# Performance work log

Hardware: AMD Instinct MI355X
Metric: run time of the kernel (lower is better)

The kernel has to match this reference:

```python
import jax, jax.numpy as jnp
import numpy as np
import math

B, S, D, H = 2, 2048, 1024, 16
DK = D // H


def setup_inputs() -> dict:
    key = jax.random.key(0)
    ks = jax.random.split(key, 12)
    s = 1.0 / math.sqrt(D)
    inp = {
        "query": jax.random.normal(ks[0], (B, S, D), jnp.float32),
        "key": jax.random.normal(ks[1], (B, S, D), jnp.float32),
        "value": jax.random.normal(ks[2], (B, S, D), jnp.float32),
        # causal mask, 0 = masked
        "mask": jnp.tril(jnp.ones((S, S), jnp.int32))[None].repeat(B, axis=0),
        "Wq": jax.random.normal(ks[3], (D, D), jnp.float32) * s,
        "bq": jnp.zeros((D,), jnp.float32),
        "Wk": jax.random.normal(ks[4], (D, D), jnp.float32) * s,
        "bk": jnp.zeros((D,), jnp.float32),
        "Wv": jax.random.normal(ks[5], (D, D), jnp.float32) * s,
        "bv": jnp.zeros((D,), jnp.float32),
        "Wo": jax.random.normal(ks[6], (D, D), jnp.float32) * s,
        "bo": jnp.zeros((D,), jnp.float32),
    }
    return inp


def _split_heads(x):
    # [B, S, D] -> [B, H, S, DK]
    b, s, _ = x.shape
    return x.reshape(b, s, H, DK).transpose(0, 2, 1, 3)


def reference(query, key, value, mask, Wq, bq, Wk, bk, Wv, bv, Wo, bo):
    q = _split_heads(query @ Wq + bq)
    k = _split_heads(key @ Wk + bk)
    v = _split_heads(value @ Wv + bv)
    scores = jnp.einsum("bhqd,bhkd->bhqk", q, k) / math.sqrt(DK)
    # mask: [B, Sq, Sk] -> broadcast over heads; 0 entries get -1e9
    scores = jnp.where(mask[:, None, :, :] == 0, jnp.float32(-1e9), scores)
    p = jax.nn.softmax(scores, axis=-1)  # dropout p=0 (eval) -> identity
    x = jnp.einsum("bhqk,bhkd->bhqd", p, v)
    x = x.transpose(0, 2, 1, 3).reshape(query.shape[0], -1, D)
    return x @ Wo + bo
```

## Files before the change

kernel.cpp:

```cpp
#include <hip/hip_runtime.h>
#include <hip/hip_bf16.h>
#include <stdint.h>


constexpr int BATCH = 2, SEQ = 2048, DIM = 1024, NH = 16, HD = 64;
constexpr int MROWS = BATCH * SEQ;

typedef __attribute__((ext_vector_type(4))) float f32x4;
typedef __attribute__((ext_vector_type(8))) short bf16x8;
typedef __attribute__((ext_vector_type(4))) int i32x4;

#define DEVI __device__ __forceinline__

DEVI ushort f2bf(float f) {
  __hip_bfloat16 h = __float2bfloat16(f);
  return __builtin_bit_cast(ushort, h);
}

DEVI f32x4 mfma16(bf16x8 a, bf16x8 b, f32x4 c) {
  return __builtin_amdgcn_mfma_f32_16x16x32_bf16(a, b, c, 0, 0, 0);
}

#if __has_builtin(__builtin_amdgcn_exp2f)
DEVI float fexp2(float x) { return __builtin_amdgcn_exp2f(x); }
#else
DEVI float fexp2(float x) { return exp2f(x); }
#endif

__global__ __launch_bounds__(256) void cvt3(const float* __restrict__ q,
                                            const float* __restrict__ k,
                                            const float* __restrict__ v,
                                            ushort* __restrict__ qo,
                                            ushort* __restrict__ ko,
                                            ushort* __restrict__ vo) {
  const float* src = blockIdx.z == 0 ? q : (blockIdx.z == 1 ? k : v);
  ushort* dst = blockIdx.z == 0 ? qo : (blockIdx.z == 1 ? ko : vo);
  int i = (blockIdx.x * 256 + threadIdx.x) * 4;
  float4 f = *(const float4*)(src + i);
  ushort4 o4 = {f2bf(f.x), f2bf(f.y), f2bf(f.z), f2bf(f.w)};
  *(ushort4*)(dst + i) = o4;
}

__global__ __launch_bounds__(256) void tw(const float* __restrict__ w0,
                                          const float* __restrict__ w1,
                                          const float* __restrict__ w2,
                                          const float* __restrict__ w3,
                                          ushort* __restrict__ t0,
                                          ushort* __restrict__ t1,
                                          ushort* __restrict__ t2,
                                          ushort* __restrict__ t3) {
  const float* W = blockIdx.z == 0 ? w0 : blockIdx.z == 1 ? w1 : blockIdx.z == 2 ? w2 : w3;
  ushort* T = blockIdx.z == 0 ? t0 : blockIdx.z == 1 ? t1 : blockIdx.z == 2 ? t2 : t3;
  __shared__ float tile[32][33];
  int k0 = blockIdx.x * 32, n0 = blockIdx.y * 32;
  int tx = threadIdx.x & 31, ty = threadIdx.x >> 5;
  #pragma unroll
  for (int i = 0; i < 32; i += 8) tile[ty + i][tx] = W[(size_t)(k0 + ty + i) * DIM + n0 + tx];
  __syncthreads();
  #pragma unroll
  for (int i = 0; i < 32; i += 8) T[(size_t)(n0 + ty + i) * DIM + k0 + tx] = f2bf(tile[tx][ty + i]);
}

struct GemmPtrs {
  const ushort* A[3];
  const ushort* Bt[3];
  const float* bias[3];
  void* C[3];
  float scale[3];
};

template <bool F32OUT, bool VT>
__global__ __launch_bounds__(256, 2) void gemm_bt(GemmPtrs gp, int M, int N, int K) {
  const int z = blockIdx.z;
  const ushort* __restrict__ A = gp.A[z];
  const ushort* __restrict__ Bt = gp.Bt[z];
  const float* __restrict__ bias = gp.bias[z];
  const float scale = gp.scale[z];
  const bool vsw = VT && (z == 2);

  __shared__ __align__(16) ushort As[2][128 * 32];
  __shared__ __align__(16) ushort Bs[2][128 * 32];

  const int tid = threadIdx.x;
  const int lane = tid & 63, wv = tid >> 6;
  const int wm = wv >> 1, wn = wv & 1;
  const int l15 = lane & 15, lg = lane >> 4;
  const int m0 = blockIdx.y * 128, n0 = blockIdx.x * 128;

  f32x4 acc[4][4];
  #pragma unroll
  for (int i = 0; i < 4; ++i)
    #pragma unroll
    for (int j = 0; j < 4; ++j) acc[i][j] = f32x4{0.f, 0.f, 0.f, 0.f};

  const int row0 = tid >> 2, k4 = tid & 3;
  const int row1 = row0 + 64;
  const size_t aoff0 = (size_t)(m0 + row0) * K + k4 * 8;
  const size_t aoff1 = (size_t)(m0 + row1) * K + k4 * 8;
  const size_t boff0 = (size_t)(n0 + row0) * K + k4 * 8;
  const size_t boff1 = (size_t)(n0 + row1) * K + k4 * 8;

  i32x4 ra0 = *(const i32x4*)(A + aoff0);
  i32x4 rb0 = *(const i32x4*)(Bt + boff0);
  i32x4 ra1 = *(const i32x4*)(A + aoff1);
  i32x4 rb1 = *(const i32x4*)(Bt + boff1);
  *(i32x4*)&As[0][(size_t)tid * 8] = ra0;
  *(i32x4*)&As[0][(size_t)(256 + tid) * 8] = ra1;
  *(i32x4*)&Bs[0][(size_t)tid * 8] = rb0;
  *(i32x4*)&Bs[0][(size_t)(256 + tid) * 8] = rb1;

  const int nk = K >> 5;
  for (int kt = 0; kt < nk; ++kt) {
    const int cur = kt & 1;
    if (kt + 1 < nk) {
      const int ko = (kt + 1) << 5;
      ra0 = *(const i32x4*)(A + aoff0 + ko);
      rb0 = *(const i32x4*)(Bt + boff0 + ko);
      ra1 = *(const i32x4*)(A + aoff1 + ko);
      rb1 = *(const i32x4*)(Bt + boff1 + ko);
    }
    __syncthreads();

    const ushort* Af = vsw ? &Bs[cur][0] : &As[cur][0];
    const ushort* Bf = vsw ? &As[cur][0] : &Bs[cur][0];
    bf16x8 af[4], bfr[4];
    #pragma unroll
    for (int i = 0; i < 4; ++i) af[i] = *(const bf16x8*)&Af[(wm * 64 + i * 16 + l15) * 32 + lg * 8];
    #pragma unroll
    for (int i = 0; i < 4; ++i) bfr[i] = *(const bf16x8*)&Bf[(wn * 64 + i * 16 + l15) * 32 + lg * 8];
    #pragma unroll
    for (int i = 0; i < 4; ++i)
      #pragma unroll
      for (int j = 0; j < 4; ++j) acc[i][j] = mfma16(af[i], bfr[j], acc[i][j]);

    if (kt + 1 < nk) {
      *(i32x4*)&As[cur ^ 1][(size_t)tid * 8] = ra0;
      *(i32x4*)&As[cur ^ 1][(size_t)(256 + tid) * 8] = ra1;
      *(i32x4*)&Bs[cur ^ 1][(size_t)tid * 8] = rb0;
      *(i32x4*)&Bs[cur ^ 1][(size_t)(256 + tid) * 8] = rb1;
    }
  }

  if (vsw) {
    ushort* Vt = (ushort*)gp.C[z];
    #pragma unroll
    for (int i = 0; i < 4; ++i)
      #pragma unroll
      for (int r = 0; r < 4; ++r) {
        int ch = n0 + wm * 64 + i * 16 + lg * 4 + r;
        float bch = bias[ch];
        int hh = ch >> 6, dch = ch & 63;
        #pragma unroll
        for (int j = 0; j < 4; ++j) {
          int tok = m0 + wn * 64 + j * 16 + l15;
          int bb = tok >> 11, s = tok & 2047;
          float val = (acc[i][j][r] + bch) * scale;
          Vt[(((size_t)bb * 16 + hh) * 64 + dch) * 2048 + s] = f2bf(val);
        }
      }
  } else {
    float bv[4];
    #pragma unroll
    for (int j = 0; j < 4; ++j) bv[j] = bias[n0 + wn * 64 + j * 16 + l15];
    #pragma unroll
    for (int i = 0; i < 4; ++i)
      #pragma unroll
      for (int j = 0; j < 4; ++j)
        #pragma unroll
        for (int r = 0; r < 4; ++r) {
          int row = m0 + wm * 64 + i * 16 + lg * 4 + r;
          int col = n0 + wn * 64 + j * 16 + l15;
          float val = (acc[i][j][r] + bv[j]) * scale;
          if (F32OUT)
            ((float*)gp.C[z])[(size_t)row * N + col] = val;
          else
            ((ushort*)gp.C[z])[(size_t)row * N + col] = f2bf(val);
        }
  }
}

__global__ __launch_bounds__(256, 3) void attn(const ushort* __restrict__ Qp,
                                               const ushort* __restrict__ Kp,
                                               const ushort* __restrict__ Vtg,
                                               ushort* __restrict__ Xb) {
  __shared__ __align__(16) ushort Kl[2][64 * 64];
  __shared__ __align__(16) ushort Vl[2][64 * 64];
  __shared__ __align__(16) ushort Pl[4][16 * 64];

  const int bh = blockIdx.x;
  const int qt = (int)gridDim.y - 1 - (int)blockIdx.y;
  const int b = bh >> 4, h = bh & 15;
  const int tid = threadIdx.x;
  const int wv = tid >> 6, lane = tid & 63;
  const int l15 = lane & 15, lg = lane >> 4;

  const size_t base = ((size_t)b * SEQ) * DIM + (size_t)h * HD;
  const ushort* Vtb = Vtg + (size_t)bh * HD * SEQ;

  const ushort* qp = Qp + base + (size_t)(qt * 64 + wv * 16 + l15) * DIM + lg * 8;
  bf16x8 qa[2] = {*(const bf16x8*)qp, *(const bf16x8*)(qp + 32)};

  f32x4 o[4];
  #pragma unroll
  for (int i = 0; i < 4; ++i) o[i] = f32x4{0.f, 0.f, 0.f, 0.f};
  float m_run[4] = {0.f, 0.f, 0.f, 0.f};
  float l_run[4] = {0.f, 0.f, 0.f, 0.f};

  const int row0 = qt * 64 + wv * 16 + lg * 4;
  const int ntiles = qt + 1;

  const int srow0 = tid >> 3, sc8 = tid & 7;
  const int srow1 = srow0 + 32;
  const int soff0 = (srow0 * 128 + sc8 * 16) ^ ((srow0 & 7) << 4);
  const int soff1 = (srow1 * 128 + sc8 * 16) ^ ((srow1 & 7) << 4);
  const ushort* Kb = Kp + base;

  i32x4 rk0 = *(const i32x4*)(Kb + (size_t)srow0 * DIM + sc8 * 8);
  i32x4 rk1 = *(const i32x4*)(Kb + (size_t)srow1 * DIM + sc8 * 8);
  i32x4 rv0 = *(const i32x4*)(Vtb + (size_t)srow0 * SEQ + sc8 * 8);
  i32x4 rv1 = *(const i32x4*)(Vtb + (size_t)srow1 * SEQ + sc8 * 8);
  *(i32x4*)((char*)&Kl[0][0] + soff0) = rk0;
  *(i32x4*)((char*)&Kl[0][0] + soff1) = rk1;
  *(i32x4*)((char*)&Vl[0][0] + soff0) = rv0;
  *(i32x4*)((char*)&Vl[0][0] + soff1) = rv1;

  for (int t = 0; t < ntiles; ++t) {
    const int cur = t & 1;
    const int kv0 = t * 64;

    if (t + 1 < ntiles) {
      const ushort* Kn = Kb + (size_t)(kv0 + 64) * DIM;
      const ushort* Vn = Vtb + (size_t)(kv0 + 64);
      rk0 = *(const i32x4*)(Kn + (size_t)srow0 * DIM + sc8 * 8);
      rk1 = *(const i32x4*)(Kn + (size_t)srow1 * DIM + sc8 * 8);
      rv0 = *(const i32x4*)(Vn + (size_t)srow0 * SEQ + sc8 * 8);
      rv1 = *(const i32x4*)(Vn + (size_t)srow1 * SEQ + sc8 * 8);
    }
    __syncthreads();

    const char* KL = (const char*)&Kl[cur][0];
    const char* VL = (const char*)&Vl[cur][0];

    f32x4 sc[4];
    #pragma unroll
    for (int n = 0; n < 4; ++n) sc[n] = f32x4{0.f, 0.f, 0.f, 0.f};
    __builtin_amdgcn_s_setprio(1);
    #pragma unroll
    for (int n = 0; n < 4; ++n) {
      int key = l15 + 16 * n;
      #pragma unroll
      for (int kc = 0; kc < 2; ++kc) {
        int off = (key * 128 + kc * 64 + lg * 16) ^ ((key & 7) << 4);
        bf16x8 kb = *(const bf16x8*)(KL + off);
        sc[n] = mfma16(qa[kc], kb, sc[n]);
      }
    }
    __builtin_amdgcn_s_setprio(0);

    if (kv0 + 63 > row0) {
      #pragma unroll
      for (int n = 0; n < 4; ++n) {
        int kcol = kv0 + l15 + 16 * n;
        #pragma unroll
        for (int r = 0; r < 4; ++r)
          if (kcol > row0 + r) sc[n][r] = -1e30f;
      }
    }

    bool big = false;
    #pragma unroll
    for (int n = 0; n < 4; ++n)
      #pragma unroll
      for (int r = 0; r < 4; ++r) big |= (sc[n][r] > m_run[r] + 8.f);
    if (__any(big)) {
      #pragma unroll
      for (int r = 0; r < 4; ++r) {
        float mx = fmaxf(fmaxf(sc[0][r], sc[1][r]), fmaxf(sc[2][r], sc[3][r]));
        mx = fmaxf(mx, __shfl_xor(mx, 1));
        mx = fmaxf(mx, __shfl_xor(mx, 2));
        mx = fmaxf(mx, __shfl_xor(mx, 4));
        mx = fmaxf(mx, __shfl_xor(mx, 8));
        float mnew = fmaxf(m_run[r], mx);
        float alpha = fexp2(m_run[r] - mnew);
        m_run[r] = mnew;
        l_run[r] *= alpha;
        #pragma unroll
        for (int nd = 0; nd < 4; ++nd) o[nd][r] *= alpha;
      }
    }
    float rsum[4] = {0.f, 0.f, 0.f, 0.f};
    #pragma unroll
    for (int n = 0; n < 4; ++n)
      #pragma unroll
      for (int r = 0; r < 4; ++r) {
        float p = fexp2(sc[n][r] - m_run[r]);
        sc[n][r] = p;
        rsum[r] += p;
      }
    #pragma unroll
    for (int r = 0; r < 4; ++r) l_run[r] += rsum[r];

    ushort* pb = &Pl[wv][0];
    #pragma unroll
    for (int n = 0; n < 4; ++n)
      #pragma unroll
      for (int r = 0; r < 4; ++r) {
        int prow = lg * 4 + r, pcol = l15 + 16 * n;
        int off = (prow * 128 + pcol * 2) ^ ((prow & 7) << 4);
        *(ushort*)((char*)pb + off) = f2bf(sc[n][r]);
      }
    bf16x8 pa[2];
    #pragma unroll
    for (int kc = 0; kc < 2; ++kc) {
      int off = (l15 * 128 + kc * 64 + lg * 16) ^ ((l15 & 7) << 4);
      pa[kc] = *(const bf16x8*)((char*)pb + off);
    }

    __builtin_amdgcn_s_setprio(1);
    #pragma unroll
    for (int kc = 0; kc < 2; ++kc)
      #pragma unroll
      for (int nd = 0; nd < 4; ++nd) {
        int vrow = nd * 16 + l15;
        int off = (vrow * 128 + kc * 64 + lg * 16) ^ ((vrow & 7) << 4);
        bf16x8 vb = *(const bf16x8*)(VL + off);
        o[nd] = mfma16(pa[kc], vb, o[nd]);
      }
    __builtin_amdgcn_s_setprio(0);

    if (t + 1 < ntiles) {
      char* KLn = (char*)&Kl[cur ^ 1][0];
      char* VLn = (char*)&Vl[cur ^ 1][0];
      *(i32x4*)(KLn + soff0) = rk0;
      *(i32x4*)(KLn + soff1) = rk1;
      *(i32x4*)(VLn + soff0) = rv0;
      *(i32x4*)(VLn + soff1) = rv1;
    }
  }

  #pragma unroll
  for (int r = 0; r < 4; ++r) {
    float s = l_run[r];
    s += __shfl_xor(s, 1);
    s += __shfl_xor(s, 2);
    s += __shfl_xor(s, 4);
    s += __shfl_xor(s, 8);
    l_run[r] = 1.0f / s;
  }
  #pragma unroll
  for (int nd = 0; nd < 4; ++nd)
    #pragma unroll
    for (int r = 0; r < 4; ++r) {
      int row = qt * 64 + wv * 16 + lg * 4 + r;
      int col = l15 + 16 * nd;
      Xb[base + (size_t)row * DIM + col] = f2bf(o[nd][r] * l_run[r]);
    }
}

extern "C" void kernel_launch(void* const* d_in, const int* in_sizes, int n_in,
                              void* d_out, int out_size, void* d_ws, size_t ws_size,
                              hipStream_t stream) {
  const float* query = (const float*)d_in[0];
  const float* keyp  = (const float*)d_in[1];
  const float* value = (const float*)d_in[2];
  const float* Wq = (const float*)d_in[4];
  const float* bq = (const float*)d_in[5];
  const float* Wk = (const float*)d_in[6];
  const float* bk = (const float*)d_in[7];
  const float* Wv = (const float*)d_in[8];
  const float* bv = (const float*)d_in[9];
  const float* Wo = (const float*)d_in[10];
  const float* bo = (const float*)d_in[11];
  float* out = (float*)d_out;

  char* w = (char*)d_ws;
  const size_t MAT = (size_t)MROWS * DIM * sizeof(ushort);
  const size_t WMT = (size_t)DIM * DIM * sizeof(ushort);
  ushort* qb  = (ushort*)w; w += MAT;
  ushort* kb  = (ushort*)w; w += MAT;
  ushort* vb  = (ushort*)w; w += MAT;
  ushort* WqT = (ushort*)w; w += WMT;
  ushort* WkT = (ushort*)w; w += WMT;
  ushort* WvT = (ushort*)w; w += WMT;
  ushort* WoT = (ushort*)w; w += WMT;
  ushort* Qp  = (ushort*)w; w += MAT;
  ushort* Kp  = (ushort*)w; w += MAT;
  ushort* Vt  = (ushort*)w; w += MAT;
  ushort* Xb  = (ushort*)w; w += MAT;

  cvt3<<<dim3(MROWS * DIM / 4 / 256, 1, 3), 256, 0, stream>>>(query, keyp, value, qb, kb, vb);
  tw<<<dim3(32, 32, 4), 256, 0, stream>>>(Wq, Wk, Wv, Wo, WqT, WkT, WvT, WoT);

  GemmPtrs g1;
  g1.A[0] = qb;  g1.A[1] = kb;  g1.A[2] = vb;
  g1.Bt[0] = WqT; g1.Bt[1] = WkT; g1.Bt[2] = WvT;
  g1.bias[0] = bq; g1.bias[1] = bk; g1.bias[2] = bv;
  g1.C[0] = Qp; g1.C[1] = Kp; g1.C[2] = Vt;
  g1.scale[0] = 0.125f * 1.4426950408889634f; g1.scale[1] = 1.f; g1.scale[2] = 1.f;
  gemm_bt<false, true><<<dim3(DIM / 128, MROWS / 128, 3), 256, 0, stream>>>(g1, MROWS, DIM, DIM);

  attn<<<dim3(BATCH * NH, SEQ / 64), 256, 0, stream>>>(Qp, Kp, Vt, Xb);

  GemmPtrs g2;
  g2.A[0] = Xb; g2.A[1] = Xb; g2.A[2] = Xb;
  g2.Bt[0] = WoT; g2.Bt[1] = WoT; g2.Bt[2] = WoT;
  g2.bias[0] = bo; g2.bias[1] = bo; g2.bias[2] = bo;
  g2.C[0] = out; g2.C[1] = out; g2.C[2] = out;
  g2.scale[0] = 1.f; g2.scale[1] = 1.f; g2.scale[2] = 1.f;
  gemm_bt<true, false><<<dim3(DIM / 128, MROWS / 128, 1), 256, 0, stream>>>(g2, MROWS, DIM, DIM);
}
```

Baseline: 121.9 us.

## Fuse fp32-to-bf16 input conversion into QKV GEMM and transpose attention MFMA operands

Removes the separate cvt3 kernel. The QKV projection GEMM now loads fp32 activations directly and converts them to bf16 while staging them into shared memory, which saves a full write and re-read of three bf16 activation copies. The attention kernel also swaps the MFMA operand order so each lane owns one query row. This makes the softmax row max and sum single scalars reduced with only two shuffles, lets P and the output be written as packed 4-element stores, and limits causal masking to the last tile. The cost is that the GEMM A-tile now reads twice as many bytes per tile and does conversion work inside its main loop.

```diff
diff --git a/kernel.cpp b/kernel.cpp
--- a/kernel.cpp
+++ b/kernel.cpp
@@ -27,18 +27,13 @@
 DEVI float fexp2(float x) { return exp2f(x); }
 #endif
 
-__global__ __launch_bounds__(256) void cvt3(const float* __restrict__ q,
-                                            const float* __restrict__ k,
-                                            const float* __restrict__ v,
-                                            ushort* __restrict__ qo,
-                                            ushort* __restrict__ ko,
-                                            ushort* __restrict__ vo) {
-  const float* src = blockIdx.z == 0 ? q : (blockIdx.z == 1 ? k : v);
-  ushort* dst = blockIdx.z == 0 ? qo : (blockIdx.z == 1 ? ko : vo);
-  int i = (blockIdx.x * 256 + threadIdx.x) * 4;
-  float4 f = *(const float4*)(src + i);
-  ushort4 o4 = {f2bf(f.x), f2bf(f.y), f2bf(f.z), f2bf(f.w)};
-  *(ushort4*)(dst + i) = o4;
+DEVI i32x4 cvt8(f32x4 a, f32x4 b) {
+  union { ushort u[8]; i32x4 v; } r;
+  #pragma unroll
+  for (int j = 0; j < 4; ++j) r.u[j] = f2bf(a[j]);
+  #pragma unroll
+  for (int j = 0; j < 4; ++j) r.u[4 + j] = f2bf(b[j]);
+  return r.v;
 }
 
 __global__ __launch_bounds__(256) void tw(const float* __restrict__ w0,
@@ -62,17 +57,18 @@
 }
 
 struct GemmPtrs {
-  const ushort* A[3];
+  const void* A[3];
   const ushort* Bt[3];
   const float* bias[3];
   void* C[3];
   float scale[3];
 };
 
-template <bool F32OUT, bool VT>
+template <bool F32OUT, bool VT, bool AF32>
 __global__ __launch_bounds__(256, 2) void gemm_bt(GemmPtrs gp, int M, int N, int K) {
   const int z = blockIdx.z;
-  const ushort* __restrict__ A = gp.A[z];
+  const float* __restrict__ A32 = (const float*)gp.A[z];
+  const ushort* __restrict__ A16 = (const ushort*)gp.A[z];
   const ushort* __restrict__ Bt = gp.Bt[z];
   const float* __restrict__ bias = gp.bias[z];
   const float scale = gp.scale[z];
@@ -100,12 +96,25 @@
   const size_t boff0 = (size_t)(n0 + row0) * K + k4 * 8;
   const size_t boff1 = (size_t)(n0 + row1) * K + k4 * 8;
 
-  i32x4 ra0 = *(const i32x4*)(A + aoff0);
-  i32x4 rb0 = *(const i32x4*)(Bt + boff0);
-  i32x4 ra1 = *(const i32x4*)(A + aoff1);
-  i32x4 rb1 = *(const i32x4*)(Bt + boff1);
-  *(i32x4*)&As[0][(size_t)tid * 8] = ra0;
-  *(i32x4*)&As[0][(size_t)(256 + tid) * 8] = ra1;
+  f32x4 fa00, fa01, fa10, fa11;
+  i32x4 ra0, ra1, rb0, rb1;
+
+  if (AF32) {
+    fa00 = *(const f32x4*)(A32 + aoff0); fa01 = *(const f32x4*)(A32 + aoff0 + 4);
+    fa10 = *(const f32x4*)(A32 + aoff1); fa11 = *(const f32x4*)(A32 + aoff1 + 4);
+  } else {
+    ra0 = *(const i32x4*)(A16 + aoff0);
+    ra1 = *(const i32x4*)(A16 + aoff1);
+  }
+  rb0 = *(const i32x4*)(Bt + boff0);
+  rb1 = *(const i32x4*)(Bt + boff1);
+  if (AF32) {
+    *(i32x4*)&As[0][(size_t)tid * 8] = cvt8(fa00, fa01);
+    *(i32x4*)&As[0][(size_t)(256 + tid) * 8] = cvt8(fa10, fa11);
+  } else {
+    *(i32x4*)&As[0][(size_t)tid * 8] = ra0;
+    *(i32x4*)&As[0][(size_t)(256 + tid) * 8] = ra1;
+  }
   *(i32x4*)&Bs[0][(size_t)tid * 8] = rb0;
   *(i32x4*)&Bs[0][(size_t)(256 + tid) * 8] = rb1;
 
@@ -114,9 +123,14 @@
     const int cur = kt & 1;
     if (kt + 1 < nk) {
       const int ko = (kt + 1) << 5;
-      ra0 = *(const i32x4*)(A + aoff0 + ko);
+      if (AF32) {
+        fa00 = *(const f32x4*)(A32 + aoff0 + ko); fa01 = *(const f32x4*)(A32 + aoff0 + ko + 4);
+        fa10 = *(const f32x4*)(A32 + aoff1 + ko); fa11 = *(const f32x4*)(A32 + aoff1 + ko + 4);
+      } else {
+        ra0 = *(const i32x4*)(A16 + aoff0 + ko);
+        ra1 = *(const i32x4*)(A16 + aoff1 + ko);
+      }
       rb0 = *(const i32x4*)(Bt + boff0 + ko);
-      ra1 = *(const i32x4*)(A + aoff1 + ko);
       rb1 = *(const i32x4*)(Bt + boff1 + ko);
     }
     __syncthreads();
@@ -134,8 +148,13 @@
       for (int j = 0; j < 4; ++j) acc[i][j] = mfma16(af[i], bfr[j], acc[i][j]);
 
     if (kt + 1 < nk) {
-      *(i32x4*)&As[cur ^ 1][(size_t)tid * 8] = ra0;
-      *(i32x4*)&As[cur ^ 1][(size_t)(256 + tid) * 8] = ra1;
+      if (AF32) {
+        *(i32x4*)&As[cur ^ 1][(size_t)tid * 8] = cvt8(fa00, fa01);
+        *(i32x4*)&As[cur ^ 1][(size_t)(256 + tid) * 8] = cvt8(fa10, fa11);
+      } else {
+        *(i32x4*)&As[cur ^ 1][(size_t)tid * 8] = ra0;
+        *(i32x4*)&As[cur ^ 1][(size_t)(256 + tid) * 8] = ra1;
+      }
       *(i32x4*)&Bs[cur ^ 1][(size_t)tid * 8] = rb0;
       *(i32x4*)&Bs[cur ^ 1][(size_t)(256 + tid) * 8] = rb1;
     }
@@ -193,20 +212,22 @@
   const int tid = threadIdx.x;
   const int wv = tid >> 6, lane = tid & 63;
   const int l15 = lane & 15, lg = lane >> 4;
+  const int swz = (l15 & 7) << 4;
 
   const size_t base = ((size_t)b * SEQ) * DIM + (size_t)h * HD;
   const ushort* Vtb = Vtg + (size_t)bh * HD * SEQ;
 
-  const ushort* qp = Qp + base + (size_t)(qt * 64 + wv * 16 + l15) * DIM + lg * 8;
+  const int qrow = qt * 64 + wv * 16 + l15;
+
+  const ushort* qp = Qp + base + (size_t)qrow * DIM + lg * 8;
   bf16x8 qa[2] = {*(const bf16x8*)qp, *(const bf16x8*)(qp + 32)};
 
   f32x4 o[4];
   #pragma unroll
   for (int i = 0; i < 4; ++i) o[i] = f32x4{0.f, 0.f, 0.f, 0.f};
-  float m_run[4] = {0.f, 0.f, 0.f, 0.f};
-  float l_run[4] = {0.f, 0.f, 0.f, 0.f};
-
-  const int row0 = qt * 64 + wv * 16 + lg * 4;
+  float m_run = 0.f;
+  float l_run = 0.f;
+
   const int ntiles = qt + 1;
 
   const int srow0 = tid >> 3, sc8 = tid & 7;
@@ -247,72 +268,62 @@
     __builtin_amdgcn_s_setprio(1);
     #pragma unroll
     for (int n = 0; n < 4; ++n) {
-      int key = l15 + 16 * n;
       #pragma unroll
       for (int kc = 0; kc < 2; ++kc) {
-        int off = (key * 128 + kc * 64 + lg * 16) ^ ((key & 7) << 4);
-        bf16x8 kb = *(const bf16x8*)(KL + off);
-        sc[n] = mfma16(qa[kc], kb, sc[n]);
+        int off = ((16 * n + l15) * 128 + kc * 64 + lg * 16) ^ swz;
+        bf16x8 kf = *(const bf16x8*)(KL + off);
+        sc[n] = mfma16(kf, qa[kc], sc[n]);
       }
     }
     __builtin_amdgcn_s_setprio(0);
 
-    if (kv0 + 63 > row0) {
+    if (t == ntiles - 1) {
       #pragma unroll
       for (int n = 0; n < 4; ++n) {
-        int kcol = kv0 + l15 + 16 * n;
+        int kb0 = kv0 + 16 * n + lg * 4;
         #pragma unroll
         for (int r = 0; r < 4; ++r)
-          if (kcol > row0 + r) sc[n][r] = -1e30f;
-      }
-    }
-
-    bool big = false;
+          if (kb0 + r > qrow) sc[n][r] = -1e30f;
+      }
+    }
+
+    float mx = sc[0][0];
     #pragma unroll
     for (int n = 0; n < 4; ++n)
       #pragma unroll
-      for (int r = 0; r < 4; ++r) big |= (sc[n][r] > m_run[r] + 8.f);
-    if (__any(big)) {
+      for (int r = 0; r < 4; ++r) mx = fmaxf(mx, sc[n][r]);
+    if (__any(mx > m_run + 8.f)) {
+      float rm = fmaxf(mx, __shfl_xor(mx, 16));
+      rm = fmaxf(rm, __shfl_xor(rm, 32));
+      float mnew = fmaxf(m_run, rm);
+      float alpha = fexp2(m_run - mnew);
+      m_run = mnew;
+      l_run *= alpha;
+      #pragma unroll
+      for (int nd = 0; nd < 4; ++nd) o[nd] *= alpha;
+    }
+    float rsum = 0.f;
+    #pragma unroll
+    for (int n = 0; n < 4; ++n)
       #pragma unroll
       for (int r = 0; r < 4; ++r) {
-        float mx = fmaxf(fmaxf(sc[0][r], sc[1][r]), fmaxf(sc[2][r], sc[3][r]));
-        mx = fmaxf(mx, __shfl_xor(mx, 1));
-        mx = fmaxf(mx, __shfl_xor(mx, 2));
-        mx = fmaxf(mx, __shfl_xor(mx, 4));
-        mx = fmaxf(mx, __shfl_xor(mx, 8));
-        float mnew = fmaxf(m_run[r], mx);
-        float alpha = fexp2(m_run[r] - mnew);
-        m_run[r] = mnew;
-        l_run[r] *= alpha;
-        #pragma unroll
-        for (int nd = 0; nd < 4; ++nd) o[nd][r] *= alpha;
-      }
-    }
-    float rsum[4] = {0.f, 0.f, 0.f, 0.f};
-    #pragma unroll
-    for (int n = 0; n < 4; ++n)
-      #pragma unroll
-      for (int r = 0; r < 4; ++r) {
-        float p = fexp2(sc[n][r] - m_run[r]);
+        float p = fexp2(sc[n][r] - m_run);
         sc[n][r] = p;
-        rsum[r] += p;
-      }
-    #pragma unroll
-    for (int r = 0; r < 4; ++r) l_run[r] += rsum[r];
+        rsum += p;
+      }
+    l_run += rsum;
 
     ushort* pb = &Pl[wv][0];
     #pragma unroll
-    for (int n = 0; n < 4; ++n)
-      #pragma unroll
-      for (int r = 0; r < 4; ++r) {
-        int prow = lg * 4 + r, pcol = l15 + 16 * n;
-        int off = (prow * 128 + pcol * 2) ^ ((prow & 7) << 4);
-        *(ushort*)((char*)pb + off) = f2bf(sc[n][r]);
-      }
+    for (int n = 0; n < 4; ++n) {
+      ushort4 pk = {f2bf(sc[n][0]), f2bf(sc[n][1]), f2bf(sc[n][2]), f2bf(sc[n][3])};
+      int off = (l15 * 128 + n * 32 + lg * 8) ^ swz;
+      *(ushort4*)((char*)pb + off) = pk;
+    }
     bf16x8 pa[2];
     #pragma unroll
     for (int kc = 0; kc < 2; ++kc) {
-      int off = (l15 * 128 + kc * 64 + lg * 16) ^ ((l15 & 7) << 4);
+      int off = (l15 * 128 + kc * 64 + lg * 16) ^ swz;
       pa[kc] = *(const bf16x8*)((char*)pb + off);
     }
 
@@ -321,10 +332,9 @@
     for (int kc = 0; kc < 2; ++kc)
       #pragma unroll
       for (int nd = 0; nd < 4; ++nd) {
-        int vrow = nd * 16 + l15;
-        int off = (vrow * 128 + kc * 64 + lg * 16) ^ ((vrow & 7) << 4);
-        bf16x8 vb = *(const bf16x8*)(VL + off);
-        o[nd] = mfma16(pa[kc], vb, o[nd]);
+        int off = ((16 * nd + l15) * 128 + kc * 64 + lg * 16) ^ swz;
+        bf16x8 vf = *(const bf16x8*)(VL + off);
+        o[nd] = mfma16(vf, pa[kc], o[nd]);
       }
     __builtin_amdgcn_s_setprio(0);
 
@@ -338,23 +348,17 @@
     }
   }
 
-  #pragma unroll
-  for (int r = 0; r < 4; ++r) {
-    float s = l_run[r];
-    s += __shfl_xor(s, 1);
-    s += __shfl_xor(s, 2);
-    s += __shfl_xor(s, 4);
-    s += __shfl_xor(s, 8);
-    l_run[r] = 1.0f / s;
-  }
-  #pragma unroll
-  for (int nd = 0; nd < 4; ++nd)
-    #pragma unroll
-    for (int r = 0; r < 4; ++r) {
-      int row = qt * 64 + wv * 16 + lg * 4 + r;
-      int col = l15 + 16 * nd;
-      Xb[base + (size_t)row * DIM + col] = f2bf(o[nd][r] * l_run[r]);
-    }
+  float s = l_run;
+  s += __shfl_xor(s, 16);
+  s += __shfl_xor(s, 32);
+  const float inv = 1.0f / s;
+  ushort* xp = Xb + base + (size_t)qrow * DIM;
+  #pragma unroll
+  for (int nd = 0; nd < 4; ++nd) {
+    ushort4 xk = {f2bf(o[nd][0] * inv), f2bf(o[nd][1] * inv),
+                  f2bf(o[nd][2] * inv), f2bf(o[nd][3] * inv)};
+    *(ushort4*)(xp + nd * 16 + lg * 4) = xk;
+  }
 }
 
 extern "C" void kernel_launch(void* const* d_in, const int* in_sizes, int n_in,
@@ -376,9 +380,6 @@
   char* w = (char*)d_ws;
   const size_t MAT = (size_t)MROWS * DIM * sizeof(ushort);
   const size_t WMT = (size_t)DIM * DIM * sizeof(ushort);
-  ushort* qb  = (ushort*)w; w += MAT;
-  ushort* kb  = (ushort*)w; w += MAT;
-  ushort* vb  = (ushort*)w; w += MAT;
   ushort* WqT = (ushort*)w; w += WMT;
   ushort* WkT = (ushort*)w; w += WMT;
   ushort* WvT = (ushort*)w; w += WMT;
@@ -388,16 +389,15 @@
   ushort* Vt  = (ushort*)w; w += MAT;
   ushort* Xb  = (ushort*)w; w += MAT;
 
-  cvt3<<<dim3(MROWS * DIM / 4 / 256, 1, 3), 256, 0, stream>>>(query, keyp, value, qb, kb, vb);
   tw<<<dim3(32, 32, 4), 256, 0, stream>>>(Wq, Wk, Wv, Wo, WqT, WkT, WvT, WoT);
 
   GemmPtrs g1;
-  g1.A[0] = qb;  g1.A[1] = kb;  g1.A[2] = vb;
+  g1.A[0] = query; g1.A[1] = keyp; g1.A[2] = value;
   g1.Bt[0] = WqT; g1.Bt[1] = WkT; g1.Bt[2] = WvT;
   g1.bias[0] = bq; g1.bias[1] = bk; g1.bias[2] = bv;
   g1.C[0] = Qp; g1.C[1] = Kp; g1.C[2] = Vt;
   g1.scale[0] = 0.125f * 1.4426950408889634f; g1.scale[1] = 1.f; g1.scale[2] = 1.f;
-  gemm_bt<false, true><<<dim3(DIM / 128, MROWS / 128, 3), 256, 0, stream>>>(g1, MROWS, DIM, DIM);
+  gemm_bt<false, true, true><<<dim3(DIM / 128, MROWS / 128, 3), 256, 0, stream>>>(g1, MROWS, DIM, DIM);
 
   attn<<<dim3(BATCH * NH, SEQ / 64), 256, 0, stream>>>(Qp, Kp, Vt, Xb);
 
@@ -407,5 +407,5 @@
   g2.bias[0] = bo; g2.bias[1] = bo; g2.bias[2] = bo;
   g2.C[0] = out; g2.C[1] = out; g2.C[2] = out;
   g2.scale[0] = 1.f; g2.scale[1] = 1.f; g2.scale[2] = 1.f;
-  gemm_bt<true, false><<<dim3(DIM / 128, MROWS / 128, 1), 256, 0, stream>>>(g2, MROWS, DIM, DIM);
-}
+  gemm_bt<true, false, false><<<dim3(DIM / 128, MROWS / 128, 1), 256, 0, stream>>>(g2, MROWS, DIM, DIM);
+}
```

New measurement: 125.2 us. 1.03x slower.
